# Kernel optimization log

Hardware: AMD Instinct MI355X
Metric: run time of the kernel (lower is better)

Reference implementation:

```python
import jax, jax.numpy as jnp
import numpy as np

N_NODES = 100000
N_EDGES = 1600000
F_IN = 128
H1 = 128
H2 = 128
N_CLASSES = 40


def setup_inputs() -> dict:
    key = jax.random.key(0)
    ks = jax.random.split(key, 8)
    node_features = jax.random.normal(ks[0], (N_NODES, F_IN), dtype=jnp.float32)
    edge_indices = jax.random.randint(ks[1], (2, N_EDGES), 0, N_NODES, dtype=jnp.int32)
    # Glorot-ish init for weights
    W1 = jax.random.normal(ks[2], (F_IN, H1), dtype=jnp.float32) / np.sqrt(F_IN)
    b1 = jnp.zeros((H1,), dtype=jnp.float32)
    W2 = jax.random.normal(ks[3], (H1, H2), dtype=jnp.float32) / np.sqrt(H1)
    b2 = jnp.zeros((H2,), dtype=jnp.float32)
    Wl = jax.random.normal(ks[4], (H2, N_CLASSES), dtype=jnp.float32) / np.sqrt(H2)
    bl = jnp.zeros((N_CLASSES,), dtype=jnp.float32)
    return {
        "node_features": node_features,
        "edge_indices": edge_indices,
        "W1": W1, "b1": b1,
        "W2": W2, "b2": b2,
        "Wl": Wl, "bl": bl,
    }


def _gcn_norm(edge_indices, n_nodes):
    # PyG GCNConv default: add self-loops, symmetric normalization.
    src = jnp.concatenate([edge_indices[0], jnp.arange(n_nodes, dtype=edge_indices.dtype)])
    dst = jnp.concatenate([edge_indices[1], jnp.arange(n_nodes, dtype=edge_indices.dtype)])
    deg = jax.ops.segment_sum(jnp.ones_like(dst, dtype=jnp.float32), dst,
                              num_segments=n_nodes)  # degree over destinations (col)
    deg_inv_sqrt = jnp.where(deg > 0, jax.lax.rsqrt(deg), 0.0)
    norm = deg_inv_sqrt[src] * deg_inv_sqrt[dst]  # (E + N,)
    return src, dst, norm


def _gcn_conv(x, W, b, src, dst, norm, n_nodes):
    xw = x @ W                                    # (N, F_out) dense GEMM
    msg = xw[src] * norm[:, None]                 # gather + scale: (E+N, F_out)
    out = jax.ops.segment_sum(msg, dst, num_segments=n_nodes)  # scatter-add
    return out + b


def reference(node_features, edge_indices, W1, b1, W2, b2, Wl, bl):
    n = node_features.shape[0]
    src, dst, norm = _gcn_norm(edge_indices, n)
    # dropout is identity in eval mode
    x = jax.nn.relu(_gcn_conv(node_features, W1, b1, src, dst, norm, n))
    x = jax.nn.relu(_gcn_conv(x, W2, b2, src, dst, norm, n))
    return x @ Wl + bl  # (N, num_classes)
```

## Files before the change

kernel.cpp:

```cpp
#include <hip/hip_runtime.h>


typedef unsigned int uint32;
typedef unsigned short u16;

#define FD 128

using short8 = __attribute__((ext_vector_type(8))) short;
using f32x4  = __attribute__((ext_vector_type(4))) float;

union U4S8 { uint4 u; short8 s; };

__device__ __forceinline__ u16 f2bf(float f) {
    uint32 u = __float_as_uint(f);
    uint32 r = ((u >> 16) & 1u) + 0x7FFFu;
    return (u16)((u + r) >> 16);
}
__device__ __forceinline__ float bf2f(u16 s) { return __uint_as_float((uint32)s << 16); }
__device__ __forceinline__ float bfLo(uint32 w) { return __uint_as_float(w << 16); }
__device__ __forceinline__ float bfHi(uint32 w) { return __uint_as_float(w & 0xFFFF0000u); }

__global__ void k_beacon(float* __restrict__ out, long long n, float val) {
    long long i = (long long)blockIdx.x * 256 + threadIdx.x;
    if (i < n) out[i] = val;
}

__global__ void k_count(const int* __restrict__ dst, int* __restrict__ cnt,
                        int* __restrict__ rank, int ne, int nn) {
    int e = blockIdx.x * 256 + threadIdx.x;
    if (e < ne) {
        int d = dst[e];
        if ((unsigned)d < (unsigned)nn) rank[e] = atomicAdd(&cnt[d], 1);
    }
}

__global__ void k_scan_a(const int* __restrict__ cnt, int* __restrict__ row_start,
                         int* __restrict__ bsum, float* __restrict__ dis, int nn) {
    __shared__ int tmp[256];
    int t = threadIdx.x;
    int i = blockIdx.x * 256 + t;
    int v = (i < nn) ? cnt[i] : 0;
    if (i < nn) dis[i] = rsqrtf((float)(v + 1));
    tmp[t] = v;
    __syncthreads();
    for (int off = 1; off < 256; off <<= 1) {
        int x = (t >= off) ? tmp[t - off] : 0;
        __syncthreads();
        tmp[t] += x;
        __syncthreads();
    }
    if (i < nn) row_start[i] = tmp[t] - v;
    if (t == 255) bsum[blockIdx.x] = tmp[255];
}

__global__ void k_scan_b(int* bsum, int nb) {
    __shared__ int tmp[512];
    __shared__ int carry;
    int t = threadIdx.x;
    if (t == 0) carry = 0;
    __syncthreads();
    for (int base = 0; base < nb; base += 512) {
        int i = base + t;
        int v = (i < nb) ? bsum[i] : 0;
        tmp[t] = v;
        __syncthreads();
        for (int off = 1; off < 512; off <<= 1) {
            int x = (t >= off) ? tmp[t - off] : 0;
            __syncthreads();
            tmp[t] += x;
            __syncthreads();
        }
        if (i < nb) bsum[i] = tmp[t] - v + carry;
        __syncthreads();
        if (t == 0) carry += tmp[511];
        __syncthreads();
    }
}

__global__ void k_scan_c(int* __restrict__ row_start, const int* __restrict__ bsum,
                         int nn, int ne) {
    int i = blockIdx.x * 256 + threadIdx.x;
    if (i < nn) row_start[i] += bsum[blockIdx.x];
    if (i == 0) row_start[nn] = ne;
}

__global__ void k_fill(const int* __restrict__ src, const int* __restrict__ dst,
                       const int* __restrict__ rank,
                       const int* __restrict__ row_start,
                       int* __restrict__ col_idx, int ne, int nn) {
    int e = blockIdx.x * 256 + threadIdx.x;
    if (e < ne) {
        int d = dst[e];
        if ((unsigned)d >= (unsigned)nn) return;
        int p = row_start[d] + rank[e];
        if ((unsigned)p < (unsigned)ne) col_idx[p] = src[e];
    }
}

template <int NOUT, bool INBF, bool OUTBF>
__global__ __launch_bounds__(256) void k_mgemm(const void* __restrict__ Ap,
                                               const float* __restrict__ W,
                                               void* __restrict__ out,
                                               const float* __restrict__ bias,
                                               const float* __restrict__ rowscale,
                                               int M) {
    constexpr int NT = (NOUT + 15) / 16;
    __shared__ uint4 Bf[4][NT][64];

    int t = threadIdx.x;
    for (int e = t; e < 4 * NT * 64; e += 256) {
        int kc = e / (NT * 64);
        int rem = e - kc * (NT * 64);
        int ct = rem >> 6;
        int l  = rem & 63;
        int k0 = kc * 32 + (l >> 4) * 8;
        int c  = ct * 16 + (l & 15);
        u16 us[8];
#pragma unroll
        for (int i = 0; i < 8; i++)
            us[i] = (c < NOUT) ? f2bf(W[(size_t)(k0 + i) * NOUT + c]) : (u16)0;
        uint4 u;
        u.x = (uint32)us[0] | ((uint32)us[1] << 16);
        u.y = (uint32)us[2] | ((uint32)us[3] << 16);
        u.z = (uint32)us[4] | ((uint32)us[5] << 16);
        u.w = (uint32)us[6] | ((uint32)us[7] << 16);
        Bf[kc][ct][l] = u;
    }
    __syncthreads();

    int lane = t & 63, wv = t >> 6;
    int r0 = blockIdx.x * 64 + wv * 16;
    if (r0 >= M) return;

    int arow = r0 + (lane & 15);
    if (arow >= M) arow = M - 1;
    U4S8 af[4];
    if (INBF) {
        const u16* A = (const u16*)Ap;
#pragma unroll
        for (int kc = 0; kc < 4; kc++)
            af[kc].u = *(const uint4*)(A + (size_t)arow * FD + kc * 32 + (lane >> 4) * 8);
    } else {
        const float* A = (const float*)Ap;
#pragma unroll
        for (int kc = 0; kc < 4; kc++) {
            const float4* s = (const float4*)(A + (size_t)arow * FD + kc * 32 + (lane >> 4) * 8);
            float4 v0 = s[0], v1 = s[1];
            uint4 u;
            u.x = (uint32)f2bf(v0.x) | ((uint32)f2bf(v0.y) << 16);
            u.y = (uint32)f2bf(v0.z) | ((uint32)f2bf(v0.w) << 16);
            u.z = (uint32)f2bf(v1.x) | ((uint32)f2bf(v1.y) << 16);
            u.w = (uint32)f2bf(v1.z) | ((uint32)f2bf(v1.w) << 16);
            af[kc].u = u;
        }
    }

    f32x4 acc[NT];
#pragma unroll
    for (int ct = 0; ct < NT; ct++) acc[ct] = f32x4{0.f, 0.f, 0.f, 0.f};
#pragma unroll
    for (int kc = 0; kc < 4; kc++) {
#pragma unroll
        for (int ct = 0; ct < NT; ct++) {
            U4S8 b;
            b.u = Bf[kc][ct][lane];
            acc[ct] = __builtin_amdgcn_mfma_f32_16x16x32_bf16(af[kc].s, b.s, acc[ct], 0, 0, 0);
        }
    }

    int rb = r0 + (lane >> 4) * 4;
    if (OUTBF) {
        uint32* yt = (uint32*)out;
#pragma unroll
        for (int r = 0; r < 4; r++) {
            int row = rb + r;
            int rc = row < M ? row : M - 1;
            float rs = rowscale ? rowscale[rc] : 1.f;
#pragma unroll
            for (int ct = 0; ct < NT; ct++) {
                float v = acc[ct][r] * rs;
                float vn = __shfl_xor(v, 1);
                if (!(lane & 1) && row < M) {
                    uint32 word = (uint32)f2bf(v) | ((uint32)f2bf(vn) << 16);
                    yt[(size_t)row * 128 + (ct * 16 + (lane & 15)) / 2] = word;
                }
            }
        }
    } else {
        float* fo = (float*)out;
#pragma unroll
        for (int r = 0; r < 4; r++) {
            int row = rb + r;
            if (row >= M) continue;
#pragma unroll
            for (int ct = 0; ct < NT; ct++) {
                int c = ct * 16 + (lane & 15);
                if (c < NOUT) {
                    float v = acc[ct][r];
                    if (bias) v += bias[c];
                    fo[(size_t)row * NOUT + c] = v;
                }
            }
        }
    }
}

__global__ __launch_bounds__(256) void k_agg(const uint32* __restrict__ yt,
                                             const float* __restrict__ dis,
                                             const int* __restrict__ row_start,
                                             const int* __restrict__ col_idx,
                                             const float* __restrict__ bias,
                                             uint32* __restrict__ outp,
                                             int nn, int ne) {
    int lane = threadIdx.x & 63;
    int wid  = threadIdx.x >> 6;
    int g    = lane >> 4;
    int sub  = lane & 15;

    float2 bq[4];
#pragma unroll
    for (int k = 0; k < 4; k++) bq[k] = *(const float2*)(bias + (sub * 4 + k) * 2);

    const int stride = gridDim.x * 16;
    for (int n0 = blockIdx.x * 16 + wid * 4; n0 < nn; n0 += stride) {
        int n = n0 + g;
        bool act = n < nn;
        int nl = act ? n : 0;

        float di = dis[nl];
        int jb = row_start[nl];
        int je = row_start[nl + 1];
        if (!act) { jb = 0; je = 0; }
        if (jb < 0) jb = 0;
        if (je > ne) je = ne;
        int deg = je - jb; if (deg < 0) deg = 0;
        int je1 = je - 1;

        uint4 sv = *(const uint4*)(yt + (size_t)nl * 128 + sub * 4);
        float a0 = bfLo(sv.x), a1 = bfHi(sv.x);
        float a2 = bfLo(sv.y), a3 = bfHi(sv.y);
        float a4 = bfLo(sv.z), a5 = bfHi(sv.z);
        float a6 = bfLo(sv.w), a7 = bfHi(sv.w);

        int m = deg;
        m = max(m, __shfl_xor(m, 16));
        m = max(m, __shfl_xor(m, 32));

        for (int base = 0; base < m; base += 8) {
            int jj = jb + base + (sub & 7);
            int jc = jj < je ? jj : je1;
            if (jc < 0) jc = 0;
            int sl = col_idx[jc];
            if ((unsigned)sl >= (unsigned)nn) sl = -1;

            int ss[8];
            float ww[8];
#pragma unroll
            for (int r = 0; r < 8; r++) {
                int s = __shfl(sl, (lane & 48) + r);
                ww[r] = (base + r < deg && s >= 0) ? 1.f : 0.f;
                ss[r] = s >= 0 ? s : 0;
            }
            uint4 uu[8];
#pragma unroll
            for (int r = 0; r < 8; r++)
                uu[r] = *(const uint4*)(yt + (size_t)ss[r] * 128 + sub * 4);
#pragma unroll
            for (int r = 0; r < 8; r++) {
                float wg = ww[r];
                a0 = fmaf(bfLo(uu[r].x), wg, a0); a1 = fmaf(bfHi(uu[r].x), wg, a1);
                a2 = fmaf(bfLo(uu[r].y), wg, a2); a3 = fmaf(bfHi(uu[r].y), wg, a3);
                a4 = fmaf(bfLo(uu[r].z), wg, a4); a5 = fmaf(bfHi(uu[r].z), wg, a5);
                a6 = fmaf(bfLo(uu[r].w), wg, a6); a7 = fmaf(bfHi(uu[r].w), wg, a7);
            }
        }

        if (act) {
            float r0 = fmaxf(fmaf(a0, di, bq[0].x), 0.f);
            float r1 = fmaxf(fmaf(a1, di, bq[0].y), 0.f);
            float r2 = fmaxf(fmaf(a2, di, bq[1].x), 0.f);
            float r3 = fmaxf(fmaf(a3, di, bq[1].y), 0.f);
            float r4 = fmaxf(fmaf(a4, di, bq[2].x), 0.f);
            float r5 = fmaxf(fmaf(a5, di, bq[2].y), 0.f);
            float r6 = fmaxf(fmaf(a6, di, bq[3].x), 0.f);
            float r7 = fmaxf(fmaf(a7, di, bq[3].y), 0.f);
            uint4 o;
            o.x = (uint32)f2bf(r0) | ((uint32)f2bf(r1) << 16);
            o.y = (uint32)f2bf(r2) | ((uint32)f2bf(r3) << 16);
            o.z = (uint32)f2bf(r4) | ((uint32)f2bf(r5) << 16);
            o.w = (uint32)f2bf(r6) | ((uint32)f2bf(r7) << 16);
            *(uint4*)(outp + (size_t)n * 64 + sub * 4) = o;
        }
    }
}

static inline char* carve(char*& p, size_t bytes) {
    char* r = p;
    p += (bytes + 255) & ~(size_t)255;
    return r;
}

extern "C" void kernel_launch(void* const* d_in, const int* in_sizes, int n_in,
                              void* d_out, int out_size, void* d_ws, size_t ws_size,
                              hipStream_t stream) {
    const long long outn = out_size;
    float* dout = (float*)d_out;
    if (n_in < 8) {
        k_beacon<<<(int)((outn + 255) / 256), 256, 0, stream>>>(dout, outn, 888.f);
        return;
    }
    float* X        = (float*)d_in[0];
    const int* ei   = (const int*)d_in[1];
    const float* W1 = (const float*)d_in[2];
    const float* b1 = (const float*)d_in[3];
    const float* W2 = (const float*)d_in[4];
    const float* b2 = (const float*)d_in[5];
    const float* Wl = (const float*)d_in[6];
    const float* bl = (const float*)d_in[7];

    const int H1 = in_sizes[3];
    const int F  = in_sizes[2] / (H1 > 0 ? H1 : 1);
    const int NC = in_sizes[7];
    const int NN = in_sizes[0] / (F > 0 ? F : 1);
    const int NE = in_sizes[1] / 2;
    if (NN <= 0 || NE <= 0 || F != FD || H1 != FD || NC != 40 ||
        (long long)NN * FD != in_sizes[0] || outn != (long long)NN * NC) {
        k_beacon<<<(int)((outn + 255) / 256), 256, 0, stream>>>(dout, outn, 888.f);
        return;
    }

    const int* src = ei;
    const int* dst = ei + NE;
    const int nb = (NN + 255) / 256;

    char* p = (char*)d_ws;
    int*   cnt       = (int*)  carve(p, (size_t)NN * 4);
    float* dis       = (float*)carve(p, (size_t)NN * 4);
    int*   bsum      = (int*)  carve(p, (size_t)nb * 4);
    int*   row_start = (int*)  carve(p, ((size_t)NN + 1) * 4);
    u16*   bufA      = (u16*)  carve(p, (size_t)NN * FD * 2);
    size_t needed = (size_t)(p - (char*)d_ws);
    bool in_out = (size_t)NE * 8 <= (size_t)outn * 4;
    int* col_idx;
    int* rank;
    if (in_out) {
        col_idx = (int*)d_out;
        rank = (int*)((char*)d_out + (size_t)NE * 4);
    } else {
        col_idx = (int*)carve(p, (size_t)NE * 4);
        rank = (int*)carve(p, (size_t)NE * 4);
        needed = (size_t)(p - (char*)d_ws);
    }
    if (needed > ws_size) {
        k_beacon<<<(int)((outn + 255) / 256), 256, 0, stream>>>(dout, outn, 999.f);
        return;
    }

    const int eb = (NE + 255) / 256;
    const int gemm_blocks = (NN + 63) / 64;
    int agg_blocks = (NN + 15) / 16;
    if (agg_blocks > 2048) agg_blocks = 2048;

    hipMemsetAsync(cnt, 0, (size_t)NN * 4, stream);
    hipMemsetAsync(col_idx, 0xFF, (size_t)NE * 4, stream);
    k_count<<<eb, 256, 0, stream>>>(dst, cnt, rank, NE, NN);
    k_scan_a<<<nb, 256, 0, stream>>>(cnt, row_start, bsum, dis, NN);
    k_scan_b<<<1, 512, 0, stream>>>(bsum, nb);
    k_scan_c<<<nb, 256, 0, stream>>>(row_start, bsum, NN, NE);
    k_fill<<<eb, 256, 0, stream>>>(src, dst, rank, row_start, col_idx, NE, NN);

    k_mgemm<128, false, true><<<gemm_blocks, 256, 0, stream>>>(X, W1, X, nullptr, dis, NN);
    k_agg<<<agg_blocks, 256, 0, stream>>>((const uint32*)X, dis, row_start, col_idx,
                                          b1, (uint32*)bufA, NN, NE);
    k_mgemm<128, true, true><<<gemm_blocks, 256, 0, stream>>>(bufA, W2, X, nullptr, dis, NN);
    k_agg<<<agg_blocks, 256, 0, stream>>>((const uint32*)X, dis, row_start, col_idx,
                                          b2, (uint32*)bufA, NN, NE);
    k_mgemm<40, true, false><<<gemm_blocks, 256, 0, stream>>>(bufA, Wl, dout, bl, nullptr, NN);
}
```

Measured before the change: 374.6 us.

## Fuse CSR fill with first GEMM in one interleaved launch and vectorize count

```diff
diff --git a/kernel.cpp b/kernel.cpp
--- a/kernel.cpp
+++ b/kernel.cpp
@@ -25,12 +25,29 @@
     if (i < n) out[i] = val;
 }
 
-__global__ void k_count(const int* __restrict__ dst, int* __restrict__ cnt,
-                        int* __restrict__ rank, int ne, int nn) {
-    int e = blockIdx.x * 256 + threadIdx.x;
-    if (e < ne) {
-        int d = dst[e];
-        if ((unsigned)d < (unsigned)nn) rank[e] = atomicAdd(&cnt[d], 1);
+__global__ __launch_bounds__(256) void k_count(const int* __restrict__ dst,
+                                               int* __restrict__ cnt,
+                                               int* __restrict__ rank,
+                                               int ne, int nn) {
+    long long base = ((long long)blockIdx.x * 256 + threadIdx.x) * 4;
+    if (base + 4 <= (long long)ne) {
+        int4 d4 = *(const int4*)(dst + base);
+        int a0 = ((unsigned)d4.x < (unsigned)nn) ? d4.x : nn;
+        int a1 = ((unsigned)d4.y < (unsigned)nn) ? d4.y : nn;
+        int a2 = ((unsigned)d4.z < (unsigned)nn) ? d4.z : nn;
+        int a3 = ((unsigned)d4.w < (unsigned)nn) ? d4.w : nn;
+        int4 r4;
+        r4.x = atomicAdd(&cnt[a0], 1);
+        r4.y = atomicAdd(&cnt[a1], 1);
+        r4.z = atomicAdd(&cnt[a2], 1);
+        r4.w = atomicAdd(&cnt[a3], 1);
+        *(int4*)(rank + base) = r4;
+    } else {
+        for (long long e = base; e < (long long)ne; e++) {
+            int d = dst[e];
+            int a = ((unsigned)d < (unsigned)nn) ? d : nn;
+            rank[e] = atomicAdd(&cnt[a], 1);
+        }
     }
 }
 
@@ -84,16 +101,121 @@
     if (i == 0) row_start[nn] = ne;
 }
 
-__global__ void k_fill(const int* __restrict__ src, const int* __restrict__ dst,
-                       const int* __restrict__ rank,
-                       const int* __restrict__ row_start,
-                       int* __restrict__ col_idx, int ne, int nn) {
-    int e = blockIdx.x * 256 + threadIdx.x;
-    if (e < ne) {
-        int d = dst[e];
-        if ((unsigned)d >= (unsigned)nn) return;
-        int p = row_start[d] + rank[e];
-        if ((unsigned)p < (unsigned)ne) col_idx[p] = src[e];
+__global__ __launch_bounds__(256) void k_fill_mgemm(
+    const float* __restrict__ A, const float* __restrict__ W,
+    uint32* __restrict__ yt, const float* __restrict__ rowscale, int M,
+    const int* __restrict__ src, const int* __restrict__ dst,
+    const int* __restrict__ rank, const int* __restrict__ row_start,
+    int* __restrict__ col_idx, int ne, int nn,
+    int nfill, int ngemm) {
+    __shared__ uint4 Bf[4][8][64];
+
+    int bid = blockIdx.x;
+    int both2 = 2 * (nfill < ngemm ? nfill : ngemm);
+    bool isfill;
+    int idx;
+    if (bid < both2) { isfill = (bid & 1) == 0; idx = bid >> 1; }
+    else { isfill = nfill > ngemm; idx = (both2 >> 1) + (bid - both2); }
+
+    int t = threadIdx.x;
+
+    if (isfill) {
+        long long base = ((long long)idx * 256 + t) * 4;
+        if (base + 4 <= (long long)ne) {
+            int4 d4 = *(const int4*)(dst + base);
+            int4 s4 = *(const int4*)(src + base);
+            int4 r4 = *(const int4*)(rank + base);
+            int dd[4] = {d4.x, d4.y, d4.z, d4.w};
+            int ss[4] = {s4.x, s4.y, s4.z, s4.w};
+            int rr[4] = {r4.x, r4.y, r4.z, r4.w};
+            int pp[4];
+#pragma unroll
+            for (int r = 0; r < 4; r++) {
+                bool ok = (unsigned)dd[r] < (unsigned)nn;
+                int dv = ok ? dd[r] : 0;
+                int p = row_start[dv] + rr[r];
+                pp[r] = ok ? p : -1;
+            }
+#pragma unroll
+            for (int r = 0; r < 4; r++)
+                if ((unsigned)pp[r] < (unsigned)ne) col_idx[pp[r]] = ss[r];
+        } else {
+            for (long long e = base; e < (long long)ne; e++) {
+                int d = dst[e];
+                if ((unsigned)d >= (unsigned)nn) continue;
+                int p = row_start[d] + rank[e];
+                if ((unsigned)p < (unsigned)ne) col_idx[p] = src[e];
+            }
+        }
+        return;
+    }
+
+    for (int e = t; e < 4 * 8 * 64; e += 256) {
+        int kc = e / (8 * 64);
+        int rem = e - kc * (8 * 64);
+        int ct = rem >> 6;
+        int l  = rem & 63;
+        int k0 = kc * 32 + (l >> 4) * 8;
+        int c  = ct * 16 + (l & 15);
+        u16 us[8];
+#pragma unroll
+        for (int i = 0; i < 8; i++) us[i] = f2bf(W[(size_t)(k0 + i) * 128 + c]);
+        uint4 u;
+        u.x = (uint32)us[0] | ((uint32)us[1] << 16);
+        u.y = (uint32)us[2] | ((uint32)us[3] << 16);
+        u.z = (uint32)us[4] | ((uint32)us[5] << 16);
+        u.w = (uint32)us[6] | ((uint32)us[7] << 16);
+        Bf[kc][ct][l] = u;
+    }
+    __syncthreads();
+
+    int lane = t & 63, wv = t >> 6;
+    int r0 = idx * 64 + wv * 16;
+    if (r0 >= M) return;
+
+    int arow = r0 + (lane & 15);
+    if (arow >= M) arow = M - 1;
+    U4S8 af[4];
+#pragma unroll
+    for (int kc = 0; kc < 4; kc++) {
+        const float4* s = (const float4*)(A + (size_t)arow * FD + kc * 32 + (lane >> 4) * 8);
+        float4 v0 = s[0], v1 = s[1];
+        uint4 u;
+        u.x = (uint32)f2bf(v0.x) | ((uint32)f2bf(v0.y) << 16);
+        u.y = (uint32)f2bf(v0.z) | ((uint32)f2bf(v0.w) << 16);
+        u.z = (uint32)f2bf(v1.x) | ((uint32)f2bf(v1.y) << 16);
+        u.w = (uint32)f2bf(v1.z) | ((uint32)f2bf(v1.w) << 16);
+        af[kc].u = u;
+    }
+
+    f32x4 acc[8];
+#pragma unroll
+    for (int ct = 0; ct < 8; ct++) acc[ct] = f32x4{0.f, 0.f, 0.f, 0.f};
+#pragma unroll
+    for (int kc = 0; kc < 4; kc++) {
+#pragma unroll
+        for (int ct = 0; ct < 8; ct++) {
+            U4S8 b;
+            b.u = Bf[kc][ct][lane];
+            acc[ct] = __builtin_amdgcn_mfma_f32_16x16x32_bf16(af[kc].s, b.s, acc[ct], 0, 0, 0);
+        }
+    }
+
+    int rb = r0 + (lane >> 4) * 4;
+#pragma unroll
+    for (int r = 0; r < 4; r++) {
+        int row = rb + r;
+        int rc = row < M ? row : M - 1;
+        float rs = rowscale[rc];
+#pragma unroll
+        for (int ct = 0; ct < 8; ct++) {
+            float v = acc[ct][r] * rs;
+            float vn = __shfl_xor(v, 1);
+            if (!(lane & 1) && row < M) {
+                uint32 word = (uint32)f2bf(v) | ((uint32)f2bf(vn) << 16);
+                yt[(size_t)row * 128 + (ct * 16 + (lane & 15)) / 2] = word;
+            }
+        }
     }
 }
 
@@ -334,7 +456,7 @@
     const int nb = (NN + 255) / 256;
 
     char* p = (char*)d_ws;
-    int*   cnt       = (int*)  carve(p, (size_t)NN * 4);
+    int*   cnt       = (int*)  carve(p, ((size_t)NN + 1) * 4);
     float* dis       = (float*)carve(p, (size_t)NN * 4);
     int*   bsum      = (int*)  carve(p, (size_t)nb * 4);
     int*   row_start = (int*)  carve(p, ((size_t)NN + 1) * 4);
@@ -356,20 +478,23 @@
         return;
     }
 
-    const int eb = (NE + 255) / 256;
+    const int ecb = (int)(((long long)NE + 1023) / 1024);
     const int gemm_blocks = (NN + 63) / 64;
     int agg_blocks = (NN + 15) / 16;
     if (agg_blocks > 2048) agg_blocks = 2048;
 
-    hipMemsetAsync(cnt, 0, (size_t)NN * 4, stream);
+    hipMemsetAsync(cnt, 0, ((size_t)NN + 1) * 4, stream);
     hipMemsetAsync(col_idx, 0xFF, (size_t)NE * 4, stream);
-    k_count<<<eb, 256, 0, stream>>>(dst, cnt, rank, NE, NN);
+    k_count<<<ecb, 256, 0, stream>>>(dst, cnt, rank, NE, NN);
     k_scan_a<<<nb, 256, 0, stream>>>(cnt, row_start, bsum, dis, NN);
     k_scan_b<<<1, 512, 0, stream>>>(bsum, nb);
     k_scan_c<<<nb, 256, 0, stream>>>(row_start, bsum, NN, NE);
-    k_fill<<<eb, 256, 0, stream>>>(src, dst, rank, row_start, col_idx, NE, NN);
-
-    k_mgemm<128, false, true><<<gemm_blocks, 256, 0, stream>>>(X, W1, X, nullptr, dis, NN);
+
+    k_fill_mgemm<<<ecb + gemm_blocks, 256, 0, stream>>>(
+        X, W1, (uint32*)X, dis, NN,
+        src, dst, rank, row_start, col_idx, NE, NN,
+        ecb, gemm_blocks);
+
     k_agg<<<agg_blocks, 256, 0, stream>>>((const uint32*)X, dis, row_start, col_idx,
                                           b1, (uint32*)bufA, NN, NE);
     k_mgemm<128, true, true><<<gemm_blocks, 256, 0, stream>>>(bufA, W2, X, nullptr, dis, NN);
```

New measurement: 382.7 us. 1.02x slower.
